# Optimization experiments

Hardware: AMD Instinct MI355X
Metric: run time of the kernel (lower is better)

The kernel has to match this reference:

```python
import jax, jax.numpy as jnp
import numpy as np

BS = 8192      # total agents (batch)
T = 8          # trajectory length
NB = 128       # number of sub-batches (crowd groups)
BLK = BS // NB # agents per group = 64
EPS = 1e-7


def setup_inputs() -> dict:
    key = jax.random.key(0)
    ks = jax.random.split(key, 7)
    x = jax.random.normal(ks[0], (BS, T, 2), dtype=jnp.float32)
    # Kaiming-ish scaled params matching nn.Linear fan-in
    W1 = jax.random.normal(ks[1], (2, 32), dtype=jnp.float32) / np.sqrt(2.0)
    b1 = jax.random.normal(ks[2], (32,), dtype=jnp.float32) * 0.01
    W2 = jax.random.normal(ks[3], (32, 64), dtype=jnp.float32) / np.sqrt(32.0)
    b2 = jax.random.normal(ks[4], (64,), dtype=jnp.float32) * 0.01
    W3 = jax.random.normal(ks[5], (64, 64), dtype=jnp.float32) / np.sqrt(64.0)
    b3 = jax.random.normal(ks[6], (64,), dtype=jnp.float32) * 0.01
    starts = jnp.arange(NB, dtype=jnp.int32) * BLK
    sub_batches = jnp.stack([starts, starts + BLK], axis=1)  # [NB, 2]
    return {"x": x, "W1": W1, "b1": b1, "W2": W2, "b2": b2,
            "W3": W3, "b3": b3, "sub_batches": sub_batches}


def reference(x, W1, b1, W2, b2, W3, b3, sub_batches):
    bs = x.shape[0]
    xt = x[:, -1]                                   # [bs, 2] last timestep
    h = jax.nn.relu(xt @ W1 + b1)                   # [bs, 32]
    h = jax.nn.relu(h @ W2 + b2)                    # [bs, 64]
    h = h @ W3 + b3                                 # [bs, 64]

    nb = sub_batches.shape[0]
    blk = bs // nb
    hb = h.reshape(nb, blk, -1)                     # [nb, blk, 64]
    attn = jnp.einsum('nid,njd->nij', hb, hb)       # [nb, blk, blk]
    # Faithful to torch: attn - attn.max(1)[0] broadcasts row-max m[j]
    # along the LAST axis (attn[i,j] - m[j]).
    m = attn.max(axis=2)                            # [nb, blk]
    e = jnp.exp(attn - m[:, None, :])
    blocks = e / (e.sum(axis=2, keepdims=True) + EPS)

    # Scatter normalized blocks onto the block diagonal of a zero bs x bs matrix
    rows = sub_batches[:, 0][:, None] + jnp.arange(blk)  # [nb, blk]
    attens = jnp.zeros((bs, bs), dtype=h.dtype)
    attens = attens.at[rows[:, :, None], rows[:, None, :]].set(blocks)
    return attens
```

## Files before the change

### kernel.cpp

```cpp
#include <hip/hip_runtime.h>

#define BS   8192
#define TT   8
#define NB   128
#define BLK  64
#define EPS  1e-7f

__global__ __launch_bounds__(512) void attn_blocks(
    const float* __restrict__ x,
    const float* __restrict__ W1, const float* __restrict__ b1,
    const float* __restrict__ W2, const float* __restrict__ b2,
    const float* __restrict__ W3, const float* __restrict__ b3,
    const int*   __restrict__ sub_batches,
    float* __restrict__ out)
{
    __shared__ __align__(16) float sW2[32 * 64];
    __shared__ __align__(16) float sW3[64 * 64];
    __shared__ __align__(16) float h1[64][36];
    __shared__ __align__(16) float h2[64][68];
    __shared__ __align__(16) float h3[64][68];
    __shared__ float sW1[2 * 32];
    __shared__ float sb1[32];
    __shared__ float sb2[64];
    __shared__ float sb3[64];
    __shared__ float mcol[64];
    __shared__ float rsum[64][8];

    const int tid   = threadIdx.x;
    const int n     = blockIdx.x;
    const int start = sub_batches[2 * n];

    if (tid < 64)                            sW1[tid] = W1[tid];
    if (tid < 32)                            sb1[tid] = b1[tid];
    for (int i = tid; i < 32 * 64; i += 512) sW2[i] = W2[i];
    if (tid >= 448)                          sb2[tid - 448] = b2[tid - 448];
    for (int i = tid; i < 64 * 64; i += 512) sW3[i] = W3[i];
    if (tid >= 384 && tid < 448)             sb3[tid - 384] = b3[tid - 384];
    __syncthreads();

    const int row = tid >> 3;
    const int l8  = tid & 7;
    const int f0  = l8 * 8;

    const int r = start + row;
    const float2 xv = *(const float2*)&x[((size_t)r * TT + (TT - 1)) * 2];

    {
        const int g0 = l8 * 4;
        #pragma unroll
        for (int f = 0; f < 4; ++f) {
            float v = fmaf(xv.x, sW1[g0 + f], fmaf(xv.y, sW1[32 + g0 + f], sb1[g0 + f]));
            h1[row][g0 + f] = fmaxf(v, 0.f);
        }
    }
    __syncthreads();

    {
        float acc[8];
        #pragma unroll
        for (int i = 0; i < 8; ++i) acc[i] = sb2[f0 + i];
        for (int k = 0; k < 32; ++k) {
            const float hk = h1[row][k];
            const float4* wp = (const float4*)&sW2[k * 64 + f0];
            #pragma unroll
            for (int c = 0; c < 2; ++c) {
                const float4 w = wp[c];
                acc[4*c+0] = fmaf(hk, w.x, acc[4*c+0]);
                acc[4*c+1] = fmaf(hk, w.y, acc[4*c+1]);
                acc[4*c+2] = fmaf(hk, w.z, acc[4*c+2]);
                acc[4*c+3] = fmaf(hk, w.w, acc[4*c+3]);
            }
        }
        #pragma unroll
        for (int c = 0; c < 2; ++c) {
            ((float4*)&h2[row][f0])[c] =
                make_float4(fmaxf(acc[4*c+0], 0.f), fmaxf(acc[4*c+1], 0.f),
                            fmaxf(acc[4*c+2], 0.f), fmaxf(acc[4*c+3], 0.f));
        }
    }
    __syncthreads();

    {
        float acc[8];
        #pragma unroll
        for (int i = 0; i < 8; ++i) acc[i] = sb3[f0 + i];
        for (int k = 0; k < 64; ++k) {
            const float hk = h2[row][k];
            const float4* wp = (const float4*)&sW3[k * 64 + f0];
            #pragma unroll
            for (int c = 0; c < 2; ++c) {
                const float4 w = wp[c];
                acc[4*c+0] = fmaf(hk, w.x, acc[4*c+0]);
                acc[4*c+1] = fmaf(hk, w.y, acc[4*c+1]);
                acc[4*c+2] = fmaf(hk, w.z, acc[4*c+2]);
                acc[4*c+3] = fmaf(hk, w.w, acc[4*c+3]);
            }
        }
        #pragma unroll
        for (int c = 0; c < 2; ++c) {
            ((float4*)&h3[row][f0])[c] =
                make_float4(acc[4*c+0], acc[4*c+1], acc[4*c+2], acc[4*c+3]);
        }
    }
    __syncthreads();

    float (*attn)[68] = h2;
    {
        float4 rv[16];
        const float4* rp = (const float4*)&h3[row][0];
        #pragma unroll
        for (int kk = 0; kk < 16; ++kk) rv[kk] = rp[kk];

        for (int jj = 0; jj < 8; ++jj) {
            const int j = f0 + jj;
            const float4* vp = (const float4*)&h3[j][0];
            float s0 = 0.f, s1 = 0.f, s2 = 0.f, s3 = 0.f;
            #pragma unroll
            for (int kk = 0; kk < 16; ++kk) {
                const float4 v = vp[kk];
                s0 = fmaf(rv[kk].x, v.x, s0);
                s1 = fmaf(rv[kk].y, v.y, s1);
                s2 = fmaf(rv[kk].z, v.z, s2);
                s3 = fmaf(rv[kk].w, v.w, s3);
            }
            attn[row][j] = (s0 + s1) + (s2 + s3);
        }
    }
    __syncthreads();

    if (tid < 64) {
        const float4* ap = (const float4*)&attn[tid][0];
        float4 m4 = ap[0];
        #pragma unroll
        for (int kk = 1; kk < 16; ++kk) {
            const float4 v = ap[kk];
            m4.x = fmaxf(m4.x, v.x); m4.y = fmaxf(m4.y, v.y);
            m4.z = fmaxf(m4.z, v.z); m4.w = fmaxf(m4.w, v.w);
        }
        mcol[tid] = fmaxf(fmaxf(m4.x, m4.y), fmaxf(m4.z, m4.w));
    }
    __syncthreads();

    {
        float ps = 0.f;
        #pragma unroll
        for (int jj = 0; jj < 8; ++jj) {
            const int j = f0 + jj;
            const float e = expf(attn[row][j] - mcol[j]);
            attn[row][j] = e;
            ps += e;
        }
        rsum[row][l8] = ps;
    }
    __syncthreads();

    float s = EPS;
    #pragma unroll
    for (int i = 0; i < 8; ++i) s += rsum[row][i];
    const float inv = 1.f / s;

    float4* ob = (float4*)(out + (size_t)(start + row) * BS + start + f0);
    #pragma unroll
    for (int c = 0; c < 2; ++c) {
        const float4 e4 = ((const float4*)&attn[row][f0])[c];
        ob[c] = make_float4(e4.x * inv, e4.y * inv, e4.z * inv, e4.w * inv);
    }
}

extern "C" void kernel_launch(void* const* d_in, const int* in_sizes, int n_in,
                              void* d_out, int out_size, void* d_ws, size_t ws_size,
                              hipStream_t stream) {
    const float* x   = (const float*)d_in[0];
    const float* W1  = (const float*)d_in[1];
    const float* b1  = (const float*)d_in[2];
    const float* W2  = (const float*)d_in[3];
    const float* b2  = (const float*)d_in[4];
    const float* W3  = (const float*)d_in[5];
    const float* b3  = (const float*)d_in[6];
    const int*   sb  = (const int*)d_in[7];
    float* out = (float*)d_out;

    hipMemsetAsync(out, 0, (size_t)BS * BS * sizeof(float), stream);

    attn_blocks<<<NB, 512, 0, stream>>>(x, W1, b1, W2, b2, W3, b3, sb, out);
}
```

Baseline: 281.9 us.

## Fuse zero-fill into the attention kernel and keep MLP activations in registers

Drops the separate full-matrix memset and launches extra workgroups in the same kernel that zero only the off-diagonal regions, so the diagonal blocks are written once. The compute workgroups raise their priority, keep h1/h2 and the score rows in registers using wave shuffles, and use shuffle reductions for the max and sum instead of shared-memory passes. The h3 shared tile gets an XOR swizzle to cut bank conflicts. The zero fill assumes contiguous 64-row diagonal blocks, matching the fixed layout of sub_batches.

Result: faster. 267.8 us (-5.0%).

```diff
diff --git a/kernel.cpp b/kernel.cpp
--- a/kernel.cpp
+++ b/kernel.cpp
@@ -3,10 +3,22 @@
 #define BS   8192
 #define TT   8
 #define NB   128
-#define BLK  64
 #define EPS  1e-7f
 
-__global__ __launch_bounds__(512) void attn_blocks(
+#define THREADS    512
+#define FILL_ITERS 8
+#define F4_PER_WG  (THREADS * FILL_ITERS)
+#define NFILL      ((BS * (BS / 4)) / F4_PER_WG)
+
+#define W1_OFF 0
+#define B1_OFF 64
+#define B2_OFF 96
+#define B3_OFF 160
+#define W2_OFF 224
+#define W3_OFF 2272
+#define SW_TOT 6368
+
+__global__ __launch_bounds__(THREADS) void attn_fused(
     const float* __restrict__ x,
     const float* __restrict__ W1, const float* __restrict__ b1,
     const float* __restrict__ W2, const float* __restrict__ b2,
@@ -14,54 +26,73 @@
     const int*   __restrict__ sub_batches,
     float* __restrict__ out)
 {
-    __shared__ __align__(16) float sW2[32 * 64];
-    __shared__ __align__(16) float sW3[64 * 64];
-    __shared__ __align__(16) float h1[64][36];
-    __shared__ __align__(16) float h2[64][68];
-    __shared__ __align__(16) float h3[64][68];
-    __shared__ float sW1[2 * 32];
-    __shared__ float sb1[32];
-    __shared__ float sb2[64];
-    __shared__ float sb3[64];
+    const int tid = threadIdx.x;
+    const int bid = blockIdx.x;
+
+    if (bid >= NB) {
+        float4* __restrict__ out4 = (float4*)out;
+        const float4 z = make_float4(0.f, 0.f, 0.f, 0.f);
+        const int base = (bid - NB) * F4_PER_WG + tid;
+        #pragma unroll
+        for (int it = 0; it < FILL_ITERS; ++it) {
+            const int idx = base + it * THREADS;
+            const int row = idx >> 11;
+            const int c4  = idx & 2047;
+            if ((c4 >> 4) != (row >> 6)) out4[idx] = z;
+        }
+        return;
+    }
+
+    __builtin_amdgcn_s_setprio(1);
+
+    __shared__ __align__(16) float sw[SW_TOT];
+    __shared__ __align__(16) float h3s[64 * 64];
     __shared__ float mcol[64];
-    __shared__ float rsum[64][8];
-
-    const int tid   = threadIdx.x;
-    const int n     = blockIdx.x;
-    const int start = sub_batches[2 * n];
-
-    if (tid < 64)                            sW1[tid] = W1[tid];
-    if (tid < 32)                            sb1[tid] = b1[tid];
-    for (int i = tid; i < 32 * 64; i += 512) sW2[i] = W2[i];
-    if (tid >= 448)                          sb2[tid - 448] = b2[tid - 448];
-    for (int i = tid; i < 64 * 64; i += 512) sW3[i] = W3[i];
-    if (tid >= 384 && tid < 448)             sb3[tid - 384] = b3[tid - 384];
+
+    const int start = sub_batches[2 * bid];
+
+    if (tid < 224) {
+        float v;
+        if      (tid < 64)  v = W1[tid];
+        else if (tid < 96)  v = b1[tid - 64];
+        else if (tid < 160) v = b2[tid - 96];
+        else                v = b3[tid - 160];
+        sw[tid] = v;
+    }
+    for (int i = tid; i < 2048; i += THREADS) sw[W2_OFF + i] = W2[i];
+    for (int i = tid; i < 4096; i += THREADS) sw[W3_OFF + i] = W3[i];
     __syncthreads();
 
-    const int row = tid >> 3;
-    const int l8  = tid & 7;
-    const int f0  = l8 * 8;
+    const int row   = tid >> 3;
+    const int l8    = tid & 7;
+    const int f0    = l8 * 8;
+    const int lane  = tid & 63;
+    const int rbase = lane & ~7;
+    const int swk   = (row >> 3) & 7;
 
     const int r = start + row;
     const float2 xv = *(const float2*)&x[((size_t)r * TT + (TT - 1)) * 2];
 
+    float h1r[4];
     {
         const int g0 = l8 * 4;
         #pragma unroll
         for (int f = 0; f < 4; ++f) {
-            float v = fmaf(xv.x, sW1[g0 + f], fmaf(xv.y, sW1[32 + g0 + f], sb1[g0 + f]));
-            h1[row][g0 + f] = fmaxf(v, 0.f);
-        }
-    }
-    __syncthreads();
-
+            float v = fmaf(xv.x, sw[W1_OFF + g0 + f],
+                     fmaf(xv.y, sw[W1_OFF + 32 + g0 + f], sw[B1_OFF + g0 + f]));
+            h1r[f] = fmaxf(v, 0.f);
+        }
+    }
+
+    float h2r[8];
     {
         float acc[8];
         #pragma unroll
-        for (int i = 0; i < 8; ++i) acc[i] = sb2[f0 + i];
+        for (int i = 0; i < 8; ++i) acc[i] = sw[B2_OFF + f0 + i];
+        #pragma unroll
         for (int k = 0; k < 32; ++k) {
-            const float hk = h1[row][k];
-            const float4* wp = (const float4*)&sW2[k * 64 + f0];
+            const float hk = __shfl(h1r[k & 3], rbase + (k >> 2));
+            const float4* wp = (const float4*)&sw[W2_OFF + k * 64 + f0];
             #pragma unroll
             for (int c = 0; c < 2; ++c) {
                 const float4 w = wp[c];
@@ -72,21 +103,17 @@
             }
         }
         #pragma unroll
-        for (int c = 0; c < 2; ++c) {
-            ((float4*)&h2[row][f0])[c] =
-                make_float4(fmaxf(acc[4*c+0], 0.f), fmaxf(acc[4*c+1], 0.f),
-                            fmaxf(acc[4*c+2], 0.f), fmaxf(acc[4*c+3], 0.f));
-        }
-    }
-    __syncthreads();
+        for (int i = 0; i < 8; ++i) h2r[i] = fmaxf(acc[i], 0.f);
+    }
 
     {
         float acc[8];
         #pragma unroll
-        for (int i = 0; i < 8; ++i) acc[i] = sb3[f0 + i];
+        for (int i = 0; i < 8; ++i) acc[i] = sw[B3_OFF + f0 + i];
+        #pragma unroll
         for (int k = 0; k < 64; ++k) {
-            const float hk = h2[row][k];
-            const float4* wp = (const float4*)&sW3[k * 64 + f0];
+            const float hk = __shfl(h2r[k & 7], rbase + (k >> 3));
+            const float4* wp = (const float4*)&sw[W3_OFF + k * 64 + f0];
             #pragma unroll
             for (int c = 0; c < 2; ++c) {
                 const float4 w = wp[c];
@@ -98,73 +125,63 @@
         }
         #pragma unroll
         for (int c = 0; c < 2; ++c) {
-            ((float4*)&h3[row][f0])[c] =
+            *(float4*)&h3s[row * 64 + (((2 * l8 + c) ^ swk) << 2)] =
                 make_float4(acc[4*c+0], acc[4*c+1], acc[4*c+2], acc[4*c+3]);
         }
     }
     __syncthreads();
 
-    float (*attn)[68] = h2;
+    float sc[8];
     {
         float4 rv[16];
-        const float4* rp = (const float4*)&h3[row][0];
-        #pragma unroll
-        for (int kk = 0; kk < 16; ++kk) rv[kk] = rp[kk];
-
+        #pragma unroll
+        for (int kk = 0; kk < 16; ++kk)
+            rv[kk] = *(const float4*)&h3s[row * 64 + ((kk ^ swk) << 2)];
+
+        #pragma unroll
         for (int jj = 0; jj < 8; ++jj) {
             const int j = f0 + jj;
-            const float4* vp = (const float4*)&h3[j][0];
+            const float* vb = &h3s[j * 64];
             float s0 = 0.f, s1 = 0.f, s2 = 0.f, s3 = 0.f;
             #pragma unroll
             for (int kk = 0; kk < 16; ++kk) {
-                const float4 v = vp[kk];
+                const float4 v = *(const float4*)&vb[(kk ^ l8) << 2];
                 s0 = fmaf(rv[kk].x, v.x, s0);
                 s1 = fmaf(rv[kk].y, v.y, s1);
                 s2 = fmaf(rv[kk].z, v.z, s2);
                 s3 = fmaf(rv[kk].w, v.w, s3);
             }
-            attn[row][j] = (s0 + s1) + (s2 + s3);
-        }
+            sc[jj] = (s0 + s1) + (s2 + s3);
+        }
+    }
+
+    {
+        float mx = sc[0];
+        #pragma unroll
+        for (int i = 1; i < 8; ++i) mx = fmaxf(mx, sc[i]);
+        mx = fmaxf(mx, __shfl_xor(mx, 1));
+        mx = fmaxf(mx, __shfl_xor(mx, 2));
+        mx = fmaxf(mx, __shfl_xor(mx, 4));
+        if (l8 == 0) mcol[row] = mx;
     }
     __syncthreads();
 
-    if (tid < 64) {
-        const float4* ap = (const float4*)&attn[tid][0];
-        float4 m4 = ap[0];
-        #pragma unroll
-        for (int kk = 1; kk < 16; ++kk) {
-            const float4 v = ap[kk];
-            m4.x = fmaxf(m4.x, v.x); m4.y = fmaxf(m4.y, v.y);
-            m4.z = fmaxf(m4.z, v.z); m4.w = fmaxf(m4.w, v.w);
-        }
-        mcol[tid] = fmaxf(fmaxf(m4.x, m4.y), fmaxf(m4.z, m4.w));
-    }
-    __syncthreads();
-
-    {
-        float ps = 0.f;
-        #pragma unroll
-        for (int jj = 0; jj < 8; ++jj) {
-            const int j = f0 + jj;
-            const float e = expf(attn[row][j] - mcol[j]);
-            attn[row][j] = e;
-            ps += e;
-        }
-        rsum[row][l8] = ps;
-    }
-    __syncthreads();
-
-    float s = EPS;
+    float e[8];
+    float ps = 0.f;
     #pragma unroll
-    for (int i = 0; i < 8; ++i) s += rsum[row][i];
-    const float inv = 1.f / s;
+    for (int jj = 0; jj < 8; ++jj) {
+        const float v = expf(sc[jj] - mcol[f0 + jj]);
+        e[jj] = v;
+        ps += v;
+    }
+    ps += __shfl_xor(ps, 1);
+    ps += __shfl_xor(ps, 2);
+    ps += __shfl_xor(ps, 4);
+    const float inv = 1.f / (ps + EPS);
 
     float4* ob = (float4*)(out + (size_t)(start + row) * BS + start + f0);
-    #pragma unroll
-    for (int c = 0; c < 2; ++c) {
-        const float4 e4 = ((const float4*)&attn[row][f0])[c];
-        ob[c] = make_float4(e4.x * inv, e4.y * inv, e4.z * inv, e4.w * inv);
-    }
+    ob[0] = make_float4(e[0] * inv, e[1] * inv, e[2] * inv, e[3] * inv);
+    ob[1] = make_float4(e[4] * inv, e[5] * inv, e[6] * inv, e[7] * inv);
 }
 
 extern "C" void kernel_launch(void* const* d_in, const int* in_sizes, int n_in,
@@ -180,7 +197,5 @@
     const int*   sb  = (const int*)d_in[7];
     float* out = (float*)d_out;
 
-    hipMemsetAsync(out, 0, (size_t)BS * BS * sizeof(float), stream);
-
-    attn_blocks<<<NB, 512, 0, stream>>>(x, W1, b1, W2, b2, W3, b3, sb, out);
+    attn_fused<<<NB + NFILL, THREADS, 0, stream>>>(x, W1, b1, W2, b2, W3, b3, sb, out);
 }
```
